# Kernel optimization log

Hardware: AMD Instinct MI355X
Metric: run time of the kernel (lower is better)

The kernel has to match this reference:

```python
import jax, jax.numpy as jnp
import numpy as np

K = 3      # fixed 3x3 kernel in module
PAD = 1    # padding=1, stride=1, dilation=1, groups=1, deformable_groups=1


def _conv2d(x, w, b=None, pad=PAD):
    out = jax.lax.conv_general_dilated(
        x, w, window_strides=(1, 1), padding=((pad, pad), (pad, pad)),
        dimension_numbers=('NCHW', 'OIHW', 'NCHW'))
    if b is not None:
        out = out + b[None, :, None, None]
    return out


def _bilinear_gather(x, py, px):
    # x: [B,C,H,W]; py,px: [B,KK,H,W] float sampling coords (zero-pad outside)
    B, C, H, W = x.shape
    y0 = jnp.floor(py)
    x0 = jnp.floor(px)
    wy1 = py - y0
    wx1 = px - x0
    wy0 = 1.0 - wy1
    wx0 = 1.0 - wx1
    y0i = y0.astype(jnp.int32)
    x0i = x0.astype(jnp.int32)
    xf = x.reshape(B, C, H * W)

    def corner(yi, xi, w):
        valid = (yi >= 0) & (yi < H) & (xi >= 0) & (xi < W)
        yc = jnp.clip(yi, 0, H - 1)
        xc = jnp.clip(xi, 0, W - 1)
        idx = (yc * W + xc).reshape(B, -1)                     # [B, KK*H*W]
        v = jnp.take_along_axis(xf, idx[:, None, :], axis=2)  # [B, C, KK*H*W]
        return v * (w * valid).reshape(B, 1, -1)

    out = (corner(y0i,     x0i,     wy0 * wx0)
         + corner(y0i,     x0i + 1, wy0 * wx1)
         + corner(y0i + 1, x0i,     wy1 * wx0)
         + corner(y0i + 1, x0i + 1, wy1 * wx1))
    KK = py.shape[1]
    return out.reshape(B, C, KK, H, W)


def _deform_forward(x, offset_w, offset_b, conv_w):
    B, C, H, W = x.shape
    # offset branch: plain 3x3 conv -> [B, 2*K*K, H, W], layout (k, (dy,dx))
    off = _conv2d(x, offset_w, offset_b).reshape(B, K * K, 2, H, W)
    ys = jnp.arange(H, dtype=x.dtype)
    xs = jnp.arange(W, dtype=x.dtype)
    ky, kx = jnp.meshgrid(jnp.arange(K), jnp.arange(K), indexing='ij')
    ky = ky.reshape(-1).astype(x.dtype)   # [9]
    kx = kx.reshape(-1).astype(x.dtype)
    # sampling coords p = p0 + p_k + offset   -> [B, 9, H, W]
    py = ys[None, None, :, None] - PAD + ky[None, :, None, None] + off[:, :, 0]
    px = xs[None, None, None, :] - PAD + kx[None, :, None, None] + off[:, :, 1]
    sampled = _bilinear_gather(x, py, px)                       # [B,C,9,H,W]
    O = conv_w.shape[0]
    return jnp.einsum('bckhw,ock->bohw', sampled, conv_w.reshape(O, C, K * K))


def setup_inputs() -> dict:
    key = jax.random.key(0)
    k1, k2, k3 = jax.random.split(key, 3)
    B, C, O, H, W = 8, 256, 256, 64, 64
    x = jax.random.normal(k1, (B, C, H, W), dtype=jnp.float32)
    # small random offset weights so learned offsets are ~ +/- 2 px
    offset_w = jax.random.normal(k2, (2 * K * K, C, K, K), dtype=jnp.float32) * 0.05
    offset_b = jnp.zeros((2 * K * K,), dtype=jnp.float32)
    conv_w = jax.random.normal(k3, (O, C, K, K), dtype=jnp.float32) * 0.02
    return {"x": x, "offset_w": offset_w, "offset_b": offset_b, "conv_w": conv_w}


def reference(x, offset_w, offset_b, conv_w):
    return _deform_forward(x, offset_w, offset_b, conv_w)
```

## Files before the change

kernel.cpp:

```cpp
#include <hip/hip_runtime.h>

using short8 = __attribute__((ext_vector_type(8))) short;
using f32x4  = __attribute__((ext_vector_type(4))) float;

__device__ inline unsigned short f2bf(float f) {
  unsigned u = __float_as_uint(f);
  u += 0x7fffu + ((u >> 16) & 1u);
  return (unsigned short)(u >> 16);
}
__device__ inline float bf2f(short s) {
  return __uint_as_float(((unsigned)(unsigned short)s) << 16);
}

__device__ inline void barrier_lgkm() {
  asm volatile("s_waitcnt lgkmcnt(0)\n\ts_barrier" ::: "memory");
}

__global__ __launch_bounds__(256) void prep_all(
    const float* __restrict__ x, const float* __restrict__ cw,
    const float* __restrict__ ow, unsigned short* __restrict__ xT,
    unsigned short* __restrict__ xTlo, unsigned short* __restrict__ wBt2,
    unsigned short* __restrict__ wOt, unsigned short* __restrict__ wOtLo) {
  __shared__ float tile[32 * 268];
  int bid = blockIdx.x, tid = threadIdx.x;
  if (bid < 1024) {
    int xh = bid & 1, y = (bid >> 1) & 63, b = bid >> 7;
    int xc = tid & 31, cq = tid >> 5;
#pragma unroll 4
    for (int i = 0; i < 32; ++i) {
      int c = i * 8 + cq;
      tile[xc * 268 + c] =
          x[(((size_t)((b << 8) + c)) << 12) + (y << 6) + xh * 32 + xc];
    }
    __syncthreads();
#pragma unroll 2
    for (int i = 0; i < 8; ++i) {
      int u = i * 256 + tid;
      int site = u >> 6, c4 = u & 63;
      float4 v = *(const float4*)(tile + site * 268 + c4 * 4);
      ushort4 hi, lo;
      hi.x = f2bf(v.x); lo.x = f2bf(v.x - bf2f(hi.x));
      hi.y = f2bf(v.y); lo.y = f2bf(v.y - bf2f(hi.y));
      hi.z = f2bf(v.z); lo.z = f2bf(v.z - bf2f(hi.z));
      hi.w = f2bf(v.w); lo.w = f2bf(v.w - bf2f(hi.w));
      size_t addr = (((size_t)((b << 12) + (y << 6) + xh * 32 + site)) << 8) + c4 * 4;
      *(ushort4*)(xT + addr) = hi;
      *(ushort4*)(xTlo + addr) = lo;
    }
  } else if (bid < 3328) {
    int e = (bid - 1024) * 256 + tid;
    int kc = e & 31, o = (e >> 5) & 255, ks = e >> 13;
    int c = (ks & 7) * 32 + kc, kt = ks >> 3;
    wBt2[e] = f2bf(cw[(size_t)(o * 256 + c) * 9 + kt]);
  } else {
    int e = (bid - 3328) * 256 + tid;
    int kc = e & 31, o = (e >> 5) & 31, ks = e >> 10;
    int c = (ks & 7) * 32 + kc, kt = ks >> 3;
    float v = (o < 18) ? ow[(size_t)(o * 256 + c) * 9 + kt] : 0.f;
    unsigned short hi = f2bf(v);
    wOt[e] = hi;
    wOtLo[e] = f2bf(v - bf2f(hi));
  }
}

__device__ inline void loadBOff2(const unsigned short* wOt, const unsigned short* wOtLo,
                                 int ks, int m16, int quad, short8* bh, short8* bl) {
  const unsigned short* bp = wOt + (ks << 10) + m16 * 32 + quad * 8;
  const unsigned short* bq = wOtLo + (ks << 10) + m16 * 32 + quad * 8;
  bh[0] = *(const short8*)bp;  bh[1] = *(const short8*)(bp + 512);
  bl[0] = *(const short8*)bq;  bl[1] = *(const short8*)(bq + 512);
}

__global__ __launch_bounds__(256) void offset_conv4(
    const unsigned short* __restrict__ xT, const unsigned short* __restrict__ xTlo,
    const unsigned short* __restrict__ wOt, const unsigned short* __restrict__ wOtLo,
    float* out) {
  __shared__ unsigned short S[4 * 2 * 7920];
  int tid = threadIdx.x, lane = tid & 63, wave = tid >> 6;
  int bid = blockIdx.x;
  int b = bid & 7, h = bid >> 3;
  int m16 = lane & 15, quad = lane >> 4;
  unsigned short* Sw = S + wave * 15840;

  {
    short8 z = (short8){0, 0, 0, 0, 0, 0, 0, 0};
    if (lane < 48) {
      int j = lane & 3, r = lane >> 2;
      int buf = r >= 6; int rr = r - buf * 6; int ky = rr >> 1, pad = rr & 1;
      int pxp = pad ? 65 : 0;
      *(short8*)(Sw + buf * 7920 + (ky * 66 + pxp) * 40 + j * 8) = z;
    }
  }

  f32x4 acc[4][2];
#pragma unroll
  for (int mt = 0; mt < 4; ++mt)
#pragma unroll
    for (int j = 0; j < 2; ++j) acc[mt][j] = (f32x4){0.f, 0.f, 0.f, 0.f};

  for (int ci = 0; ci < 2; ++ci) {
    int cc = wave + ci * 4;
#pragma unroll
    for (int ky = 0; ky < 3; ++ky) {
      int y = h + ky - 1;
      unsigned short* dh = Sw + (ky * 66 + lane + 1) * 40;
      unsigned short* dl = dh + 7920;
      if ((unsigned)y < 64u) {
        size_t base = (((size_t)((b << 12) + (y << 6) + lane)) << 8) + cc * 32;
        const unsigned short* sh_ = xT + base;
        const unsigned short* sl_ = xTlo + base;
#pragma unroll
        for (int j = 0; j < 4; ++j) {
          *(short8*)(dh + j * 8) = *(const short8*)(sh_ + j * 8);
          *(short8*)(dl + j * 8) = *(const short8*)(sl_ + j * 8);
        }
      } else {
        short8 z = (short8){0, 0, 0, 0, 0, 0, 0, 0};
#pragma unroll
        for (int j = 0; j < 4; ++j) {
          *(short8*)(dh + j * 8) = z;
          *(short8*)(dl + j * 8) = z;
        }
      }
    }
    for (int kt = 0; kt < 9; ++kt) {
      int ky = kt / 3, kx = kt - ky * 3;
      short8 bh[2], bl[2];
      loadBOff2(wOt, wOtLo, kt * 8 + cc, m16, quad, bh, bl);
#pragma unroll
      for (int mt = 0; mt < 4; ++mt) {
        const unsigned short* ap = Sw + (ky * 66 + mt * 16 + m16 + kx) * 40 + quad * 8;
        short8 ah = *(const short8*)ap;
        short8 al = *(const short8*)(ap + 7920);
#pragma unroll
        for (int j = 0; j < 2; ++j) {
          acc[mt][j] = __builtin_amdgcn_mfma_f32_16x16x32_bf16(ah, bh[j], acc[mt][j], 0, 0, 0);
          acc[mt][j] = __builtin_amdgcn_mfma_f32_16x16x32_bf16(al, bh[j], acc[mt][j], 0, 0, 0);
          acc[mt][j] = __builtin_amdgcn_mfma_f32_16x16x32_bf16(ah, bl[j], acc[mt][j], 0, 0, 0);
        }
      }
    }
  }

  __syncthreads();
  float* red = (float*)S;
#pragma unroll
  for (int mt = 0; mt < 4; ++mt)
#pragma unroll
    for (int j = 0; j < 2; ++j)
      *(f32x4*)(red + ((((wave * 4 + mt) * 2) + j) * 64 + lane) * 4) = acc[mt][j];
  __syncthreads();
#pragma unroll
  for (int j = 0; j < 2; ++j) {
    int o = j * 16 + m16;
    f32x4 s = (f32x4){0.f, 0.f, 0.f, 0.f};
#pragma unroll
    for (int wv = 0; wv < 4; ++wv) {
      f32x4 v = *(const f32x4*)(red + ((((wv * 4 + wave) * 2) + j) * 64 + lane) * 4);
      s[0] += v[0]; s[1] += v[1]; s[2] += v[2]; s[3] += v[3];
    }
    if (o < 18) {
      float* po = out + (((size_t)((b << 8) + 100 + o)) << 12) + (h << 6) +
                  wave * 16 + quad * 4;
      *(float4*)po = make_float4(s[0], s[1], s[2], s[3]);
    }
  }
}

__device__ inline void gather4(const unsigned short* __restrict__ xT,
                               int bbase, int q, int jt,
                               const int2* cif2, const float4* cwf4,
                               int px, short8* g, float4& wq) {
  int cc = jt / 9, kt = jt - cc * 9;
  int2 si = cif2[kt * 64 + px];
  wq = cwf4[kt * 64 + px];
  const unsigned short* base = xT + (size_t)(unsigned)(bbase + cc * 32 + q * 8);
  g[0] = *(const short8*)(base + si.x);
  g[1] = *(const short8*)(base + si.x + 256);
  g[2] = *(const short8*)(base + si.y);
  g[3] = *(const short8*)(base + si.y + 256);
}
__device__ inline void loadB(const unsigned short* __restrict__ wBt2, int wave,
                             int m16, int quad, int jt, short8* bf) {
  int cc = jt / 9, kt = jt - cc * 9;
  int ks = kt * 8 + cc;
  const unsigned short* bp =
      wBt2 + ((size_t)ks << 13) + (wave << 11) + m16 * 32 + quad * 8;
#pragma unroll
  for (int j = 0; j < 4; ++j)
    bf[j] = *(const short8*)(bp + j * 512);
}

__global__ __launch_bounds__(256, 2) void deform_main(
    const unsigned short* __restrict__ xT, const float* __restrict__ offb,
    const unsigned short* __restrict__ wBt2, float* out) {
  __shared__ float4 smem4[1504];
  char* smem = (char*)smem4;
  float4* cwf4 = (float4*)smem;
  int2*   cif2 = (int2*)(smem + 9216);
  unsigned short* At = (unsigned short*)(smem + 13824);

  int tid = threadIdx.x, lane = tid & 63, wave = tid >> 6;
  int b = blockIdx.x & 7, h = blockIdx.x >> 3;

  size_t bb = ((size_t)(b << 8)) << 12;
  for (int it = tid; it < 576; it += 256) {
    int k = it >> 6, px = it & 63;
    int ky = k / 3, kx = k - ky * 3;
    int idx = (h << 6) + px;
    float dy = offb[2 * k]     + out[bb + (((size_t)(100 + 2 * k)) << 12) + idx];
    float dx = offb[2 * k + 1] + out[bb + (((size_t)(101 + 2 * k)) << 12) + idx];
    float py = (float)(h - 1 + ky) + dy;
    float pxx = (float)(px - 1 + kx) + dx;
    float y0f = floorf(py), x0f = floorf(pxx);
    int y0 = (int)y0f, x0 = (int)x0f;
    float wy1 = py - y0f, wx1 = pxx - x0f;
    int xb; float wxl, wxr;
    if (x0 >= 0 && x0 <= 62)      { xb = x0; wxl = 1.f - wx1; wxr = wx1; }
    else if (x0 == -1)            { xb = 0;  wxl = wx1;       wxr = 0.f; }
    else if (x0 == 63)            { xb = 62; wxl = 0.f;       wxr = 1.f - wx1; }
    else                          { xb = 0;  wxl = 0.f;       wxr = 0.f; }
    float wy0v = ((unsigned)y0 < 64u) ? (1.f - wy1) : 0.f;
    float wy1v = ((unsigned)(y0 + 1) < 64u) ? wy1 : 0.f;
    int yc0 = min(max(y0, 0), 63), yc1 = min(max(y0 + 1, 0), 63);
    cwf4[it] = make_float4(wy0v * wxl, wy0v * wxr, wy1v * wxl, wy1v * wxr);
    cif2[it] = make_int2(((yc0 << 6) + xb) << 8, ((yc1 << 6) + xb) << 8);
  }
  __syncthreads();

  int m16 = lane & 15, quad = lane >> 4;
  int px = wave * 16 + (lane >> 2);
  int q  = lane & 3;
  int bbase = b << 20;
  f32x4 acc[4][4];
#pragma unroll
  for (int i = 0; i < 4; ++i)
#pragma unroll
    for (int j = 0; j < 4; ++j) acc[i][j] = (f32x4){0.f, 0.f, 0.f, 0.f};

  short8 g[4]; float4 wq; short8 bcur[4];
  gather4(xT, bbase, q, 0, cif2, cwf4, px, g, wq);
  loadB(wBt2, wave, m16, quad, 0, bcur);

  for (int it = 0; it < 72; ++it) {
    int buf = it & 1;
    short8 av;
#pragma unroll
    for (int i = 0; i < 8; ++i) {
      float v = wq.x * bf2f(g[0][i]) + wq.y * bf2f(g[1][i]) +
                wq.z * bf2f(g[2][i]) + wq.w * bf2f(g[3][i]);
      av[i] = (short)f2bf(v);
    }
    *(short8*)(At + buf * 2560 + px * 40 + q * 8) = av;
    int jn = (it < 71) ? it + 1 : 71;
    short8 bnext[4], gn[4]; float4 wqn;
    loadB(wBt2, wave, m16, quad, jn, bnext);
    gather4(xT, bbase, q, jn, cif2, cwf4, px, gn, wqn);
    barrier_lgkm();
    short8 af[4];
#pragma unroll
    for (int mt = 0; mt < 4; ++mt)
      af[mt] = *(const short8*)(At + buf * 2560 + (mt * 16 + m16) * 40 + quad * 8);
#pragma unroll
    for (int mt = 0; mt < 4; ++mt)
#pragma unroll
      for (int j = 0; j < 4; ++j)
        acc[mt][j] = __builtin_amdgcn_mfma_f32_16x16x32_bf16(af[mt], bcur[j],
                                                             acc[mt][j], 0, 0, 0);
#pragma unroll
    for (int i = 0; i < 4; ++i) g[i] = gn[i];
    wq = wqn;
#pragma unroll
    for (int j = 0; j < 4; ++j) bcur[j] = bnext[j];
  }

#pragma unroll
  for (int j = 0; j < 4; ++j) {
    int o = wave * 64 + j * 16 + m16;
    float* po = out + (((size_t)((b << 8) + o)) << 12) + (h << 6) + quad * 4;
#pragma unroll
    for (int mt = 0; mt < 4; ++mt) {
      float4 v = make_float4(acc[mt][j][0], acc[mt][j][1], acc[mt][j][2],
                             acc[mt][j][3]);
      *(float4*)(po + mt * 16) = v;
    }
  }
}

extern "C" void kernel_launch(void* const* d_in, const int* in_sizes, int n_in,
                              void* d_out, int out_size, void* d_ws, size_t ws_size,
                              hipStream_t stream) {
  const float* x     = (const float*)d_in[0];
  const float* offw  = (const float*)d_in[1];
  const float* offb  = (const float*)d_in[2];
  const float* convw = (const float*)d_in[3];
  float* out = (float*)d_out;

  char* ws = (char*)d_ws;
  unsigned short* wOt   = (unsigned short*)ws;
  unsigned short* wOtLo = (unsigned short*)(ws + 147456);
  unsigned short* wBt2  = (unsigned short*)(ws + 294912);
  unsigned short* xT    = (unsigned short*)(ws + 1474560);
  unsigned short* xTlo  = (unsigned short*)(ws + 18251776);

  prep_all<<<3616, 256, 0, stream>>>(x, convw, offw, xT, xTlo, wBt2, wOt, wOtLo);
  offset_conv4<<<512, 256, 0, stream>>>(xT, xTlo, wOt, wOtLo, out);
  deform_main<<<512, 256, 0, stream>>>(xT, offb, wBt2, out);
}
```

Before: 189.5 us.

## Split offset conv across channel-group blocks and restructure x transpose prep

The offset convolution kernel changes from one 256-thread block that reduces four channel-group waves through shared memory to four separate 64-thread blocks. Each block writes its partial sums to its own scratch slice of the output buffer, and deform_main sums the four partials when it reads the offsets. This removes the shared-memory reduction and barriers and gives four times more, smaller blocks, at the cost of more scratch traffic and extra loads in deform_main. Separately, the x transpose in prep_all now reads a full row per thread with float4 loads, packs the hi and lo bf16 halves into one shared word, and writes 16-byte vectors.

```diff
diff --git a/kernel.cpp b/kernel.cpp
--- a/kernel.cpp
+++ b/kernel.cpp
@@ -21,39 +21,49 @@
     const float* __restrict__ ow, unsigned short* __restrict__ xT,
     unsigned short* __restrict__ xTlo, unsigned short* __restrict__ wBt2,
     unsigned short* __restrict__ wOt, unsigned short* __restrict__ wOtLo) {
-  __shared__ float tile[32 * 268];
+  __shared__ unsigned int T[64 * 268];
   int bid = blockIdx.x, tid = threadIdx.x;
-  if (bid < 1024) {
-    int xh = bid & 1, y = (bid >> 1) & 63, b = bid >> 7;
-    int xc = tid & 31, cq = tid >> 5;
+  if (bid < 512) {
+    int y = bid & 63, b = bid >> 6;
+    int c = tid;
+    const float* xp = x + (((size_t)((b << 8) + c)) << 12) + (y << 6);
+    int colp = c + 4 * (c >> 6);
 #pragma unroll 4
-    for (int i = 0; i < 32; ++i) {
-      int c = i * 8 + cq;
-      tile[xc * 268 + c] =
-          x[(((size_t)((b << 8) + c)) << 12) + (y << 6) + xh * 32 + xc];
+    for (int p4 = 0; p4 < 16; ++p4) {
+      float4 v = *(const float4*)(xp + p4 * 4);
+      float vv[4] = {v.x, v.y, v.z, v.w};
+#pragma unroll
+      for (int i = 0; i < 4; ++i) {
+        unsigned short hi = f2bf(vv[i]);
+        unsigned short lo = f2bf(vv[i] - bf2f(hi));
+        T[(p4 * 4 + i) * 268 + colp] = ((unsigned)lo << 16) | hi;
+      }
     }
     __syncthreads();
+    int px2 = tid & 63, cq = tid >> 6;
+    size_t gbase = (((size_t)((b << 12) + (y << 6) + px2)) << 8) + cq * 64;
 #pragma unroll 2
-    for (int i = 0; i < 8; ++i) {
-      int u = i * 256 + tid;
-      int site = u >> 6, c4 = u & 63;
-      float4 v = *(const float4*)(tile + site * 268 + c4 * 4);
-      ushort4 hi, lo;
-      hi.x = f2bf(v.x); lo.x = f2bf(v.x - bf2f(hi.x));
-      hi.y = f2bf(v.y); lo.y = f2bf(v.y - bf2f(hi.y));
-      hi.z = f2bf(v.z); lo.z = f2bf(v.z - bf2f(hi.z));
-      hi.w = f2bf(v.w); lo.w = f2bf(v.w - bf2f(hi.w));
-      size_t addr = (((size_t)((b << 12) + (y << 6) + xh * 32 + site)) << 8) + c4 * 4;
-      *(ushort4*)(xT + addr) = hi;
-      *(ushort4*)(xTlo + addr) = lo;
-    }
-  } else if (bid < 3328) {
-    int e = (bid - 1024) * 256 + tid;
+    for (int j = 0; j < 8; ++j) {
+      const unsigned* tp = T + px2 * 268 + cq * 68 + j * 8;
+      uint4 u0 = *(const uint4*)tp;
+      uint4 u1 = *(const uint4*)(tp + 4);
+      unsigned uu[8] = {u0.x, u0.y, u0.z, u0.w, u1.x, u1.y, u1.z, u1.w};
+      short8 hv, lv;
+#pragma unroll
+      for (int k = 0; k < 8; ++k) {
+        hv[k] = (short)(uu[k] & 0xffffu);
+        lv[k] = (short)(uu[k] >> 16);
+      }
+      *(short8*)(xT + gbase + j * 8) = hv;
+      *(short8*)(xTlo + gbase + j * 8) = lv;
+    }
+  } else if (bid < 2816) {
+    int e = (bid - 512) * 256 + tid;
     int kc = e & 31, o = (e >> 5) & 255, ks = e >> 13;
     int c = (ks & 7) * 32 + kc, kt = ks >> 3;
     wBt2[e] = f2bf(cw[(size_t)(o * 256 + c) * 9 + kt]);
   } else {
-    int e = (bid - 3328) * 256 + tid;
+    int e = (bid - 2816) * 256 + tid;
     int kc = e & 31, o = (e >> 5) & 31, ks = e >> 10;
     int c = (ks & 7) * 32 + kc, kt = ks >> 3;
     float v = (o < 18) ? ow[(size_t)(o * 256 + c) * 9 + kt] : 0.f;
@@ -71,16 +81,15 @@
   bl[0] = *(const short8*)bq;  bl[1] = *(const short8*)(bq + 512);
 }
 
-__global__ __launch_bounds__(256) void offset_conv4(
+__global__ __launch_bounds__(64) void offset_conv5(
     const unsigned short* __restrict__ xT, const unsigned short* __restrict__ xTlo,
     const unsigned short* __restrict__ wOt, const unsigned short* __restrict__ wOtLo,
     float* out) {
-  __shared__ unsigned short S[4 * 2 * 7920];
-  int tid = threadIdx.x, lane = tid & 63, wave = tid >> 6;
+  __shared__ unsigned short S[15840];
+  int lane = threadIdx.x;
   int bid = blockIdx.x;
-  int b = bid & 7, h = bid >> 3;
+  int b = bid & 7, h = (bid >> 3) & 63, cp = bid >> 9;
   int m16 = lane & 15, quad = lane >> 4;
-  unsigned short* Sw = S + wave * 15840;
 
   {
     short8 z = (short8){0, 0, 0, 0, 0, 0, 0, 0};
@@ -88,7 +97,7 @@
       int j = lane & 3, r = lane >> 2;
       int buf = r >= 6; int rr = r - buf * 6; int ky = rr >> 1, pad = rr & 1;
       int pxp = pad ? 65 : 0;
-      *(short8*)(Sw + buf * 7920 + (ky * 66 + pxp) * 40 + j * 8) = z;
+      *(short8*)(S + buf * 7920 + (ky * 66 + pxp) * 40 + j * 8) = z;
     }
   }
 
@@ -99,11 +108,11 @@
     for (int j = 0; j < 2; ++j) acc[mt][j] = (f32x4){0.f, 0.f, 0.f, 0.f};
 
   for (int ci = 0; ci < 2; ++ci) {
-    int cc = wave + ci * 4;
+    int cc = cp + ci * 4;
 #pragma unroll
     for (int ky = 0; ky < 3; ++ky) {
       int y = h + ky - 1;
-      unsigned short* dh = Sw + (ky * 66 + lane + 1) * 40;
+      unsigned short* dh = S + (ky * 66 + lane + 1) * 40;
       unsigned short* dl = dh + 7920;
       if ((unsigned)y < 64u) {
         size_t base = (((size_t)((b << 12) + (y << 6) + lane)) << 8) + cc * 32;
@@ -129,7 +138,7 @@
       loadBOff2(wOt, wOtLo, kt * 8 + cc, m16, quad, bh, bl);
 #pragma unroll
       for (int mt = 0; mt < 4; ++mt) {
-        const unsigned short* ap = Sw + (ky * 66 + mt * 16 + m16 + kx) * 40 + quad * 8;
+        const unsigned short* ap = S + (ky * 66 + mt * 16 + m16 + kx) * 40 + quad * 8;
         short8 ah = *(const short8*)ap;
         short8 al = *(const short8*)(ap + 7920);
 #pragma unroll
@@ -142,27 +151,16 @@
     }
   }
 
-  __syncthreads();
-  float* red = (float*)S;
-#pragma unroll
-  for (int mt = 0; mt < 4; ++mt)
-#pragma unroll
-    for (int j = 0; j < 2; ++j)
-      *(f32x4*)(red + ((((wave * 4 + mt) * 2) + j) * 64 + lane) * 4) = acc[mt][j];
-  __syncthreads();
 #pragma unroll
   for (int j = 0; j < 2; ++j) {
     int o = j * 16 + m16;
-    f32x4 s = (f32x4){0.f, 0.f, 0.f, 0.f};
-#pragma unroll
-    for (int wv = 0; wv < 4; ++wv) {
-      f32x4 v = *(const f32x4*)(red + ((((wv * 4 + wave) * 2) + j) * 64 + lane) * 4);
-      s[0] += v[0]; s[1] += v[1]; s[2] += v[2]; s[3] += v[3];
-    }
     if (o < 18) {
-      float* po = out + (((size_t)((b << 8) + 100 + o)) << 12) + (h << 6) +
-                  wave * 16 + quad * 4;
-      *(float4*)po = make_float4(s[0], s[1], s[2], s[3]);
+      float* po = out + (((size_t)((b << 8) + 100 + cp * 18 + o)) << 12) + (h << 6);
+#pragma unroll
+      for (int mt = 0; mt < 4; ++mt)
+#pragma unroll
+        for (int rr = 0; rr < 4; ++rr)
+          po[mt * 16 + quad * 4 + rr] = acc[mt][j][rr];
     }
   }
 }
@@ -208,8 +206,12 @@
     int k = it >> 6, px = it & 63;
     int ky = k / 3, kx = k - ky * 3;
     int idx = (h << 6) + px;
-    float dy = offb[2 * k]     + out[bb + (((size_t)(100 + 2 * k)) << 12) + idx];
-    float dx = offb[2 * k + 1] + out[bb + (((size_t)(101 + 2 * k)) << 12) + idx];
+    float dy = offb[2 * k], dx = offb[2 * k + 1];
+#pragma unroll
+    for (int g2 = 0; g2 < 4; ++g2) {
+      dy += out[bb + (((size_t)(100 + g2 * 18 + 2 * k)) << 12) + idx];
+      dx += out[bb + (((size_t)(101 + g2 * 18 + 2 * k)) << 12) + idx];
+    }
     float py = (float)(h - 1 + ky) + dy;
     float pxx = (float)(px - 1 + kx) + dx;
     float y0f = floorf(py), x0f = floorf(pxx);
@@ -303,7 +305,7 @@
   unsigned short* xT    = (unsigned short*)(ws + 1474560);
   unsigned short* xTlo  = (unsigned short*)(ws + 18251776);
 
-  prep_all<<<3616, 256, 0, stream>>>(x, convw, offw, xT, xTlo, wBt2, wOt, wOtLo);
-  offset_conv4<<<512, 256, 0, stream>>>(xT, xTlo, wOt, wOtLo, out);
+  prep_all<<<3104, 256, 0, stream>>>(x, convw, offw, xT, xTlo, wBt2, wOt, wOtLo);
+  offset_conv5<<<2048, 64, 0, stream>>>(xT, xTlo, wOt, wOtLo, out);
   deform_main<<<512, 256, 0, stream>>>(xT, offb, wBt2, out);
 }
```

After: 197.9 us. 4.5% more time.

## Fuse offset convolution into deform_main kernel via shared-memory offsets

Applied to the files above, without the earlier changes.

Removes the separate offset_conv4 launch. Each deform_main block now computes its own row of 18 offset channels with MFMA, staging the x rows through shared memory one channel chunk at a time with barriers, and keeps the offsets in LDS rather than writing them to and reading them back from the output buffer. This saves a kernel launch and the global round trip. In exchange, shared memory per block grows from about 24 KB to about 46 KB, which may reduce occupancy, and the offset conv now runs serially with per-chunk barriers before the main gather.

```diff
diff --git a/kernel.cpp b/kernel.cpp
--- a/kernel.cpp
+++ b/kernel.cpp
@@ -71,102 +71,6 @@
   bl[0] = *(const short8*)bq;  bl[1] = *(const short8*)(bq + 512);
 }
 
-__global__ __launch_bounds__(256) void offset_conv4(
-    const unsigned short* __restrict__ xT, const unsigned short* __restrict__ xTlo,
-    const unsigned short* __restrict__ wOt, const unsigned short* __restrict__ wOtLo,
-    float* out) {
-  __shared__ unsigned short S[4 * 2 * 7920];
-  int tid = threadIdx.x, lane = tid & 63, wave = tid >> 6;
-  int bid = blockIdx.x;
-  int b = bid & 7, h = bid >> 3;
-  int m16 = lane & 15, quad = lane >> 4;
-  unsigned short* Sw = S + wave * 15840;
-
-  {
-    short8 z = (short8){0, 0, 0, 0, 0, 0, 0, 0};
-    if (lane < 48) {
-      int j = lane & 3, r = lane >> 2;
-      int buf = r >= 6; int rr = r - buf * 6; int ky = rr >> 1, pad = rr & 1;
-      int pxp = pad ? 65 : 0;
-      *(short8*)(Sw + buf * 7920 + (ky * 66 + pxp) * 40 + j * 8) = z;
-    }
-  }
-
-  f32x4 acc[4][2];
-#pragma unroll
-  for (int mt = 0; mt < 4; ++mt)
-#pragma unroll
-    for (int j = 0; j < 2; ++j) acc[mt][j] = (f32x4){0.f, 0.f, 0.f, 0.f};
-
-  for (int ci = 0; ci < 2; ++ci) {
-    int cc = wave + ci * 4;
-#pragma unroll
-    for (int ky = 0; ky < 3; ++ky) {
-      int y = h + ky - 1;
-      unsigned short* dh = Sw + (ky * 66 + lane + 1) * 40;
-      unsigned short* dl = dh + 7920;
-      if ((unsigned)y < 64u) {
-        size_t base = (((size_t)((b << 12) + (y << 6) + lane)) << 8) + cc * 32;
-        const unsigned short* sh_ = xT + base;
-        const unsigned short* sl_ = xTlo + base;
-#pragma unroll
-        for (int j = 0; j < 4; ++j) {
-          *(short8*)(dh + j * 8) = *(const short8*)(sh_ + j * 8);
-          *(short8*)(dl + j * 8) = *(const short8*)(sl_ + j * 8);
-        }
-      } else {
-        short8 z = (short8){0, 0, 0, 0, 0, 0, 0, 0};
-#pragma unroll
-        for (int j = 0; j < 4; ++j) {
-          *(short8*)(dh + j * 8) = z;
-          *(short8*)(dl + j * 8) = z;
-        }
-      }
-    }
-    for (int kt = 0; kt < 9; ++kt) {
-      int ky = kt / 3, kx = kt - ky * 3;
-      short8 bh[2], bl[2];
-      loadBOff2(wOt, wOtLo, kt * 8 + cc, m16, quad, bh, bl);
-#pragma unroll
-      for (int mt = 0; mt < 4; ++mt) {
-        const unsigned short* ap = Sw + (ky * 66 + mt * 16 + m16 + kx) * 40 + quad * 8;
-        short8 ah = *(const short8*)ap;
-        short8 al = *(const short8*)(ap + 7920);
-#pragma unroll
-        for (int j = 0; j < 2; ++j) {
-          acc[mt][j] = __builtin_amdgcn_mfma_f32_16x16x32_bf16(ah, bh[j], acc[mt][j], 0, 0, 0);
-          acc[mt][j] = __builtin_amdgcn_mfma_f32_16x16x32_bf16(al, bh[j], acc[mt][j], 0, 0, 0);
-          acc[mt][j] = __builtin_amdgcn_mfma_f32_16x16x32_bf16(ah, bl[j], acc[mt][j], 0, 0, 0);
-        }
-      }
-    }
-  }
-
-  __syncthreads();
-  float* red = (float*)S;
-#pragma unroll
-  for (int mt = 0; mt < 4; ++mt)
-#pragma unroll
-    for (int j = 0; j < 2; ++j)
-      *(f32x4*)(red + ((((wave * 4 + mt) * 2) + j) * 64 + lane) * 4) = acc[mt][j];
-  __syncthreads();
-#pragma unroll
-  for (int j = 0; j < 2; ++j) {
-    int o = j * 16 + m16;
-    f32x4 s = (f32x4){0.f, 0.f, 0.f, 0.f};
-#pragma unroll
-    for (int wv = 0; wv < 4; ++wv) {
-      f32x4 v = *(const f32x4*)(red + ((((wv * 4 + wave) * 2) + j) * 64 + lane) * 4);
-      s[0] += v[0]; s[1] += v[1]; s[2] += v[2]; s[3] += v[3];
-    }
-    if (o < 18) {
-      float* po = out + (((size_t)((b << 8) + 100 + o)) << 12) + (h << 6) +
-                  wave * 16 + quad * 4;
-      *(float4*)po = make_float4(s[0], s[1], s[2], s[3]);
-    }
-  }
-}
-
 __device__ inline void gather4(const unsigned short* __restrict__ xT,
                                int bbase, int q, int jt,
                                const int2* cif2, const float4* cwf4,
@@ -192,24 +96,92 @@
 }
 
 __global__ __launch_bounds__(256, 2) void deform_main(
-    const unsigned short* __restrict__ xT, const float* __restrict__ offb,
-    const unsigned short* __restrict__ wBt2, float* out) {
-  __shared__ float4 smem4[1504];
+    const unsigned short* __restrict__ xT, const unsigned short* __restrict__ xTlo,
+    const unsigned short* __restrict__ wOt, const unsigned short* __restrict__ wOtLo,
+    const float* __restrict__ offb, const unsigned short* __restrict__ wBt2,
+    float* out) {
+  __shared__ float4 smem4[2908];
   char* smem = (char*)smem4;
+  unsigned short* S = (unsigned short*)smem;
+  float* convO = (float*)(smem + 31680);
   float4* cwf4 = (float4*)smem;
   int2*   cif2 = (int2*)(smem + 9216);
-  unsigned short* At = (unsigned short*)(smem + 13824);
+  unsigned short* At = (unsigned short*)(smem + 36288);
 
   int tid = threadIdx.x, lane = tid & 63, wave = tid >> 6;
   int b = blockIdx.x & 7, h = blockIdx.x >> 3;
-
-  size_t bb = ((size_t)(b << 8)) << 12;
+  int m16 = lane & 15, quad = lane >> 4;
+
+  {
+    short8 z = (short8){0, 0, 0, 0, 0, 0, 0, 0};
+    if (tid < 48) {
+      int j = tid & 3, r = tid >> 2;
+      int buf = r >= 6; int rr = r - buf * 6; int ky = rr >> 1, pad = rr & 1;
+      int pxp = pad ? 65 : 0;
+      *(short8*)(S + buf * 7920 + (ky * 66 + pxp) * 40 + j * 8) = z;
+    }
+  }
+  f32x4 oacc[2];
+  oacc[0] = (f32x4){0.f, 0.f, 0.f, 0.f};
+  oacc[1] = (f32x4){0.f, 0.f, 0.f, 0.f};
+
+  for (int cc = 0; cc < 8; ++cc) {
+    if (tid < 192) {
+      int ky = tid >> 6, spx = tid & 63;
+      int y = h + ky - 1;
+      unsigned short* dh = S + (ky * 66 + spx + 1) * 40;
+      unsigned short* dl = dh + 7920;
+      if ((unsigned)y < 64u) {
+        size_t base = (((size_t)((b << 12) + (y << 6) + spx)) << 8) + cc * 32;
+        const unsigned short* sh_ = xT + base;
+        const unsigned short* sl_ = xTlo + base;
+#pragma unroll
+        for (int j = 0; j < 4; ++j) {
+          *(short8*)(dh + j * 8) = *(const short8*)(sh_ + j * 8);
+          *(short8*)(dl + j * 8) = *(const short8*)(sl_ + j * 8);
+        }
+      } else {
+        short8 z = (short8){0, 0, 0, 0, 0, 0, 0, 0};
+#pragma unroll
+        for (int j = 0; j < 4; ++j) {
+          *(short8*)(dh + j * 8) = z;
+          *(short8*)(dl + j * 8) = z;
+        }
+      }
+    }
+    __syncthreads();
+    for (int kt = 0; kt < 9; ++kt) {
+      int ky = kt / 3, kx = kt - ky * 3;
+      short8 bh[2], bl[2];
+      loadBOff2(wOt, wOtLo, kt * 8 + cc, m16, quad, bh, bl);
+      const unsigned short* ap = S + (ky * 66 + wave * 16 + m16 + kx) * 40 + quad * 8;
+      short8 ah = *(const short8*)ap;
+      short8 al = *(const short8*)(ap + 7920);
+#pragma unroll
+      for (int j = 0; j < 2; ++j) {
+        oacc[j] = __builtin_amdgcn_mfma_f32_16x16x32_bf16(ah, bh[j], oacc[j], 0, 0, 0);
+        oacc[j] = __builtin_amdgcn_mfma_f32_16x16x32_bf16(al, bh[j], oacc[j], 0, 0, 0);
+        oacc[j] = __builtin_amdgcn_mfma_f32_16x16x32_bf16(ah, bl[j], oacc[j], 0, 0, 0);
+      }
+    }
+    __syncthreads();
+  }
+#pragma unroll
+  for (int j = 0; j < 2; ++j) {
+    int o = j * 16 + m16;
+    if (o < 18) {
+#pragma unroll
+      for (int rr = 0; rr < 4; ++rr)
+        convO[o * 64 + wave * 16 + quad * 4 + rr] = oacc[j][rr];
+    }
+  }
+  __syncthreads();
+
   for (int it = tid; it < 576; it += 256) {
     int k = it >> 6, px = it & 63;
     int ky = k / 3, kx = k - ky * 3;
-    int idx = (h << 6) + px;
-    float dy = offb[2 * k]     + out[bb + (((size_t)(100 + 2 * k)) << 12) + idx];
-    float dx = offb[2 * k + 1] + out[bb + (((size_t)(101 + 2 * k)) << 12) + idx];
+    float dy = offb[2 * k]     + convO[(2 * k) * 64 + px];
+    float dx = offb[2 * k + 1] + convO[(2 * k + 1) * 64 + px];
     float py = (float)(h - 1 + ky) + dy;
     float pxx = (float)(px - 1 + kx) + dx;
     float y0f = floorf(py), x0f = floorf(pxx);
@@ -228,7 +200,6 @@
   }
   __syncthreads();
 
-  int m16 = lane & 15, quad = lane >> 4;
   int px = wave * 16 + (lane >> 2);
   int q  = lane & 3;
   int bbase = b << 20;
@@ -304,6 +275,5 @@
   unsigned short* xTlo  = (unsigned short*)(ws + 18251776);
 
   prep_all<<<3616, 256, 0, stream>>>(x, convw, offw, xT, xTlo, wBt2, wOt, wOtLo);
-  offset_conv4<<<512, 256, 0, stream>>>(xT, xTlo, wOt, wOtLo, out);
-  deform_main<<<512, 256, 0, stream>>>(xT, offb, wBt2, out);
-}
+  deform_main<<<512, 256, 0, stream>>>(xT, xTlo, wOt, wOtLo, offb, wBt2, out);
+}
```

New measurement: 201.2 us. 1.06x slower.
